# Kernel optimization log

Measured on AMD Instinct MI355X. Metric: run time of the kernel, lower is better.

Reference implementation:

```python
import jax, jax.numpy as jnp
import numpy as np

DIM = 768
NUM_HEADS = 12
HEAD_DIM = DIM // NUM_HEADS
SCALE = HEAD_DIM ** -0.5


def setup_inputs() -> dict:
    key = jax.random.key(0)
    ks = jax.random.split(key, 9)
    B, L, C = 4, 1024, DIM
    x = jax.random.normal(ks[0], (B, L, C), jnp.float32)
    q_ape = jax.random.normal(ks[1], (1, L, C), jnp.float32)
    k_ape = jax.random.normal(ks[2], (1, L, C), jnp.float32)
    attn_pos = jax.random.normal(ks[3], (1, NUM_HEADS, L, L), jnp.float32)
    s = C ** -0.5
    # torch Linear weights: (out_features, in_features)
    Wq = jax.random.normal(ks[4], (C, C), jnp.float32) * s
    Wk = jax.random.normal(ks[5], (C, C), jnp.float32) * s
    Wv = jax.random.normal(ks[6], (C, C), jnp.float32) * s
    Wp = jax.random.normal(ks[7], (C, C), jnp.float32) * s
    bp = jax.random.normal(ks[8], (C,), jnp.float32) * 0.01
    return {"x": x, "q_ape": q_ape, "k_ape": k_ape, "attn_pos": attn_pos,
            "Wq": Wq, "Wk": Wk, "Wv": Wv, "Wp": Wp, "bp": bp}


def _split_heads(t):
    # (B, L, C) -> (B, H, L, D)
    B, L, C = t.shape
    return t.reshape(B, L, NUM_HEADS, HEAD_DIM).transpose(0, 2, 1, 3)


def reference(x, q_ape, k_ape, attn_pos, Wq, Wk, Wv, Wp, bp):
    B, L, C = x.shape
    q = _split_heads((x + q_ape) @ Wq.T)          # (B,H,L,D)
    k = _split_heads((x + k_ape) @ Wk.T)          # (B,H,L,D)
    v = _split_heads(x @ Wv.T)                    # (B,H,L,D)
    attn = jnp.einsum('bhqd,bhkd->bhqk', q, k) * SCALE + attn_pos
    attn = jax.nn.softmax(attn, axis=-1)
    out = jnp.einsum('bhqk,bhkd->bhqd', attn, v)  # (B,H,L,D)
    out = out.transpose(0, 2, 1, 3).reshape(B, L, C)
    return out @ Wp.T + bp
```

## Files before the change

### kernel.cpp

```cpp
#include <hip/hip_runtime.h>
#include <stdint.h>

#define NH 12
#define HD 64
#define NB 4
#define SEQ 1024
#define CDIM 768
#define MTOT (NB*SEQ)
#define MC   (MTOT*CDIM)
#define LC   (SEQ*CDIM)
#define WSZ  (CDIM*CDIM)
#define LST  104
#define EST  136
#define VST  72
#define L2E  1.44269504f
#define BHSZ (SEQ*HD)
#define PTSZ ((size_t)NH*SEQ*SEQ)

typedef __attribute__((ext_vector_type(4))) float f32x4;
typedef __attribute__((ext_vector_type(8))) __bf16 bf16x8;
typedef __attribute__((ext_vector_type(8))) short short8;
typedef __attribute__((ext_vector_type(4))) unsigned short ushort4v;
typedef unsigned short u16;

static __device__ __forceinline__ f32x4 mfma16(short8 a, short8 b, f32x4 c) {
  return __builtin_amdgcn_mfma_f32_16x16x32_bf16(
      __builtin_bit_cast(bf16x8, a), __builtin_bit_cast(bf16x8, b), c, 0, 0, 0);
}
static __device__ __forceinline__ u16 f2bf(float f) {
  unsigned u = __float_as_uint(f);
  u += 0x7FFFu + ((u >> 16) & 1u);
  return (u16)(u >> 16);
}
static __device__ __forceinline__ float bf2f(u16 h) {
  return __uint_as_float(((unsigned)h) << 16);
}
static __device__ __forceinline__ void lds_load16(const void* g, void* l) {
  __builtin_amdgcn_global_load_lds(
      (const __attribute__((address_space(1))) void*)g,
      (__attribute__((address_space(3))) void*)l, 16, 0, 0);
}

#define PREP_BLKS (MC / 4 / 256)
#define CONV_N4   ((4 * WSZ + CDIM) / 4)
#define CONV_BLKS ((CONV_N4 + 255) / 256)
__global__ __launch_bounds__(256) void prep_all(
    const float* __restrict__ xp, const float* __restrict__ qp,
    const float* __restrict__ kp, const float* __restrict__ Wq,
    const float* __restrict__ Wk, const float* __restrict__ Wv,
    const float* __restrict__ Wp, const float* __restrict__ bp,
    u16* __restrict__ Xq, u16* __restrict__ Xk, u16* __restrict__ Xv,
    u16* __restrict__ Wb) {
  int bid = blockIdx.x;
  if (bid < PREP_BLKS) {
    int i4 = bid * 256 + threadIdx.x;
    int a4 = i4 % (LC / 4);
    f32x4 xx = ((const f32x4*)xp)[i4];
    f32x4 qq = ((const f32x4*)qp)[a4];
    f32x4 kk = ((const f32x4*)kp)[a4];
    ushort4v oq, ok, ov;
#pragma unroll
    for (int j = 0; j < 4; j++) {
      oq[j] = f2bf(xx[j] + qq[j]);
      ok[j] = f2bf(xx[j] + kk[j]);
      ov[j] = f2bf(xx[j]);
    }
    ((ushort4v*)Xq)[i4] = oq;
    ((ushort4v*)Xk)[i4] = ok;
    ((ushort4v*)Xv)[i4] = ov;
  } else {
    int i4 = (bid - PREP_BLKS) * 256 + threadIdx.x;
    if (i4 >= CONV_N4) return;
    int sel = i4 / (WSZ / 4);
    int off = i4 - sel * (WSZ / 4);
    const float* src = sel == 0 ? Wq : sel == 1 ? Wk : sel == 2 ? Wv
                     : sel == 3 ? Wp : bp;
    f32x4 v = ((const f32x4*)src)[off];
    ushort4v o;
#pragma unroll
    for (int j = 0; j < 4; j++) o[j] = f2bf(v[j]);
    ((ushort4v*)Wb)[i4] = o;
  }
}

static __device__ __forceinline__ void gemm_core64(
    const u16* __restrict__ Ab, const u16* __restrict__ Wb,
    short* As, short* Bs, f32x4 acc[2][4]) {
  const int t = threadIdx.x;
  const int lane = t & 63, w = t >> 6, quad = lane >> 4, l16 = lane & 15;
  const int wm = (w >> 1) * 32, wn = (w & 1) * 64;
  const int row4 = t >> 2, chunk = (t & 3) * 8;
  for (int k0 = 0; k0 < CDIM; k0 += 64) {
#pragma unroll
    for (int hh = 0; hh < 2; hh++) {
      const u16* ga = Ab + row4 * CDIM + k0 + hh * 32 + chunk;
      const u16* gb = Wb + row4 * CDIM + k0 + hh * 32 + chunk;
      lds_load16(ga,             (char*)As + hh * 4096 + t * 16);
      lds_load16(gb,             (char*)Bs + hh * 8192 + t * 16);
      lds_load16(gb + 64 * CDIM, (char*)Bs + hh * 8192 + 4096 + t * 16);
    }
    __syncthreads();
#pragma unroll
    for (int hh = 0; hh < 2; hh++) {
      const short* Ah = As + hh * 2048;
      const short* Bh = Bs + hh * 4096;
      short8 af[2], bw[4];
#pragma unroll
      for (int i = 0; i < 2; i++)
        af[i] = *(const short8*)(Ah + (wm + i * 16 + l16) * 32 + quad * 8);
#pragma unroll
      for (int j = 0; j < 4; j++)
        bw[j] = *(const short8*)(Bh + (wn + j * 16 + l16) * 32 + quad * 8);
#pragma unroll
      for (int i = 0; i < 2; i++)
#pragma unroll
        for (int j = 0; j < 4; j++)
          acc[i][j] = mfma16(af[i], bw[j], acc[i][j]);
    }
    __syncthreads();
  }
}

__global__ __launch_bounds__(256) void gemm_qkv(
    const u16* __restrict__ Xq, const u16* __restrict__ Xk, const u16* __restrict__ Xv,
    const u16* __restrict__ Wq, const u16* __restrict__ Wk, const u16* __restrict__ Wv,
    u16* __restrict__ Q, u16* __restrict__ K, u16* __restrict__ Vt,
    const float* __restrict__ pos, u16* __restrict__ posT) {
  __shared__ __align__(16) short S[12288];
  const int id = blockIdx.x;
  const int rq = id & 3, qd = id >> 2;
  if (rq == 3) {
    const int t = threadIdx.x, wv = t >> 6, lane = t & 63;
    const int quad = lane >> 4, l16 = lane & 15;
#pragma unroll 1
    for (int c = 0; c < 8; ++c) {
      const int chunk = qd * 32 + wv * 8 + c;
      const int h = chunk >> 10, rem = chunk & 1023;
      const int rb = rem >> 4, kt = rem & 15;
      const float* src = pos + (size_t)h * SEQ * SEQ
                         + (size_t)(rb * 16 + quad * 4) * SEQ + kt * 64 + l16;
      short8 s0, s1;
#pragma unroll
      for (int jj = 0; jj < 2; jj++)
#pragma unroll
        for (int r = 0; r < 4; r++) {
          s0[jj * 4 + r] = (short)f2bf(src[r * SEQ + jj * 16] * L2E);
          s1[jj * 4 + r] = (short)f2bf(src[r * SEQ + (jj + 2) * 16] * L2E);
        }
      u16* dst = posT + (size_t)chunk * 1024 + lane * 16;
      *(short8*)dst = s0;
      *(short8*)(dst + 8) = s1;
    }
    return;
  }

  short* As = S;
  short* Bs = S + 4096;
  const int g = qd * 3 + rq;
  const int z = g / 384, rem = g % 384;
  const int m0 = (rem / 6) * 64, n0 = (rem % 6) * 128;
  const u16* A = (z == 0 ? Xq : z == 1 ? Xk : Xv) + m0 * CDIM;
  const u16* W = (z == 0 ? Wq : z == 1 ? Wk : Wv) + n0 * CDIM;
  f32x4 acc[2][4];
#pragma unroll
  for (int i = 0; i < 2; i++)
#pragma unroll
    for (int j = 0; j < 4; j++) acc[i][j] = 0.f;
  gemm_core64(A, W, As, Bs, acc);

  const int t = threadIdx.x, lane = t & 63, w = t >> 6;
  const int quad = lane >> 4, l16 = lane & 15;
  const int wm = (w >> 1) * 32, wn = (w & 1) * 64;
  const float qs = (z == 0) ? 0.125f : 1.0f;

#pragma unroll
  for (int i = 0; i < 2; i++)
#pragma unroll
    for (int j = 0; j < 4; j++)
#pragma unroll
      for (int r = 0; r < 4; r++) {
        int mr = wm + i * 16 + quad * 4 + r;
        int nc = wn + j * 16 + l16;
        if (z < 2) S[mr * EST + nc] = (short)f2bf(acc[i][j][r] * qs);
        else       S[nc * VST + mr] = (short)f2bf(acc[i][j][r]);
      }
  __syncthreads();

  const int row = t >> 3, ch = t & 7;
  const int b = m0 >> 10, lbase = m0 & 1023;
  if (z == 0) {
#pragma unroll
    for (int cp = 0; cp < 2; cp++) {
      int h = (n0 >> 6) + cp;
#pragma unroll
      for (int rp = 0; rp < 2; rp++) {
        int mr = row + rp * 32;
        short8 v = *(const short8*)(S + mr * EST + cp * 64 + ch * 8);
        *(short8*)(Q + ((((size_t)(b * NH + h)) << 10) + lbase + mr) * HD + ch * 8) = v;
      }
    }
  } else if (z == 1) {
#pragma unroll
    for (int cp = 0; cp < 2; cp++) {
      int h = (n0 >> 6) + cp;
      u16* Kp = K + (size_t)(b * NH + h) * BHSZ;
#pragma unroll
      for (int rp = 0; rp < 2; rp++) {
        int mr = row + rp * 32;
        int tok = lbase + mr;
        short8 v = *(const short8*)(S + mr * EST + cp * 64 + ch * 8);
        *(short8*)(Kp + (((tok >> 4) * 8 + ch) * 16 + (tok & 15)) * 8) = v;
      }
    }
  } else {
#pragma unroll
    for (int rp = 0; rp < 4; rp++) {
      int rn = row + rp * 32;
      int h = (n0 + rn) >> 6, d = rn & 63;
      u16* Vp = Vt + (size_t)(b * NH + h) * BHSZ;
      int jv = d >> 4, ld16 = d & 15;
      int tok = lbase + ch * 8;
      short8 v = *(const short8*)(S + rn * VST + ch * 8);
      *(short8*)(Vp + ((((tok >> 6) * 4 + jv) * 8 + ((tok >> 3) & 7)) * 16 + ld16) * 8) = v;
    }
  }
}

__global__ __launch_bounds__(256, 3) void attn(
    const u16* __restrict__ Q, const u16* __restrict__ Kf, const u16* __restrict__ Vf,
    const u16* __restrict__ posT, u16* __restrict__ O) {
  __shared__ __align__(16) short Ps[4 * 16 * LST];
  const int t = threadIdx.x, lane = t & 63, w = t >> 6;
  const int quad = lane >> 4, l16 = lane & 15;

  const int lid = blockIdx.x;
  const int k8 = lid & 7, m = lid >> 3;
  const int g = k8 * 24 + (m >> 2), b = m & 3;
  const int h = g >> 4, qt = g & 15;
  const int bh = b * NH + h;
  const int q0 = qt * 64 + w * 16;

  const u16* Kg = Kf + (size_t)bh * BHSZ;
  const u16* Vg = Vf + (size_t)bh * BHSZ;
  const u16* Tg = posT + ((size_t)(h * 1024 + (qt * 4 + w) * 16)) * 1024
                  + lane * 16;
  short* Pw = Ps + w * 16 * LST;
  const int fo = quad * 128 + l16 * 8;

  const u16* Qg = Q + ((size_t)bh * SEQ + q0) * HD;
  const short8 qa0 = *(const short8*)(Qg + l16 * HD + quad * 8);
  const short8 qa1 = *(const short8*)(Qg + l16 * HD + 32 + quad * 8);

  f32x4 o[4];
  float lrow[4];
#pragma unroll
  for (int j = 0; j < 4; j++) o[j] = 0.f;
#pragma unroll
  for (int r = 0; r < 4; r++) lrow[r] = 0.f;

  short8 kb0[4], kb1[4];
  short8 pt0, pt1;
#pragma unroll
  for (int j = 0; j < 4; j++) {
    kb0[j] = *(const short8*)(Kg + j * 1024 + fo);
    kb1[j] = *(const short8*)(Kg + j * 1024 + 512 + fo);
  }
  pt0 = *(const short8*)(Tg);
  pt1 = *(const short8*)(Tg + 8);

#pragma unroll 1
  for (int kt = 0; kt < 16; ++kt) {
    const int kbase = kt * 4096;
    short8 vb0[4], vb1[4];
#pragma unroll
    for (int j = 0; j < 4; j++) {
      vb0[j] = *(const short8*)(Vg + kbase + j * 1024 + fo);
      vb1[j] = *(const short8*)(Vg + kbase + j * 1024 + 512 + fo);
    }
    f32x4 s[4];
#pragma unroll
    for (int j = 0; j < 4; j++) {
      f32x4 zz = 0.f;
      s[j] = mfma16(qa1, kb1[j], mfma16(qa0, kb0[j], zz));
    }
#pragma unroll
    for (int j = 0; j < 2; j++)
#pragma unroll
      for (int r = 0; r < 4; r++) {
        float pv = bf2f((u16)pt0[j * 4 + r]);
        float e = __builtin_amdgcn_exp2f(fmaf(s[j][r], L2E, pv));
        unsigned bits = __float_as_uint(e);
        Pw[(quad * 4 + r) * LST + j * 16 + l16] = (short)(bits >> 16);
        lrow[r] += __uint_as_float(bits & 0xFFFF0000u);
      }
#pragma unroll
    for (int j = 2; j < 4; j++)
#pragma unroll
      for (int r = 0; r < 4; r++) {
        float pv = bf2f((u16)pt1[(j - 2) * 4 + r]);
        float e = __builtin_amdgcn_exp2f(fmaf(s[j][r], L2E, pv));
        unsigned bits = __float_as_uint(e);
        Pw[(quad * 4 + r) * LST + j * 16 + l16] = (short)(bits >> 16);
        lrow[r] += __uint_as_float(bits & 0xFFFF0000u);
      }
    if (kt < 15) {
      const int nb = kbase + 4096;
#pragma unroll
      for (int j = 0; j < 4; j++) {
        kb0[j] = *(const short8*)(Kg + nb + j * 1024 + fo);
        kb1[j] = *(const short8*)(Kg + nb + j * 1024 + 512 + fo);
      }
      pt0 = *(const short8*)(Tg + (kt + 1) * 1024);
      pt1 = *(const short8*)(Tg + (kt + 1) * 1024 + 8);
    }
    const short8 pa0 = *(const short8*)(Pw + l16 * LST + quad * 8);
    const short8 pa1 = *(const short8*)(Pw + l16 * LST + 32 + quad * 8);
#pragma unroll
    for (int j = 0; j < 4; j++)
      o[j] = mfma16(pa1, vb1[j], mfma16(pa0, vb0[j], o[j]));
  }

#pragma unroll
  for (int off = 1; off < 16; off <<= 1)
#pragma unroll
    for (int r = 0; r < 4; r++) lrow[r] += __shfl_xor(lrow[r], off);

  u16* Og = O + ((size_t)b * SEQ + q0) * CDIM + h * HD;
  float inv[4];
#pragma unroll
  for (int r = 0; r < 4; r++) inv[r] = 1.0f / lrow[r];
#pragma unroll
  for (int j = 0; j < 4; j++)
#pragma unroll
    for (int r = 0; r < 4; r++)
      Og[(quad * 4 + r) * CDIM + j * 16 + l16] = f2bf(o[j][r] * inv[r]);
}

__global__ __launch_bounds__(256) void gemm_proj(
    const u16* __restrict__ Oin, const u16* __restrict__ Wp,
    const u16* __restrict__ bp, float* __restrict__ out) {
  __shared__ __align__(16) short As[4096], Bs[4096];
  const int t = threadIdx.x;
  const int lane = t & 63, w = t >> 6, quad = lane >> 4, l16 = lane & 15;
  const int wm = (w >> 1) * 32, wn = (w & 1) * 32;
  const int row4 = t >> 2, chunk = (t & 3) * 8;
  const int m0 = blockIdx.y * 64, n0 = blockIdx.x * 64;
  const u16* Ab = Oin + m0 * CDIM;
  const u16* Wb = Wp + n0 * CDIM;
  f32x4 acc[2][2];
#pragma unroll
  for (int i = 0; i < 2; i++)
#pragma unroll
    for (int j = 0; j < 2; j++) acc[i][j] = 0.f;

  for (int k0 = 0; k0 < CDIM; k0 += 64) {
#pragma unroll
    for (int hh = 0; hh < 2; hh++) {
      const u16* ga = Ab + row4 * CDIM + k0 + hh * 32 + chunk;
      const u16* gb = Wb + row4 * CDIM + k0 + hh * 32 + chunk;
      lds_load16(ga, (char*)As + hh * 4096 + t * 16);
      lds_load16(gb, (char*)Bs + hh * 4096 + t * 16);
    }
    __syncthreads();
#pragma unroll
    for (int hh = 0; hh < 2; hh++) {
      const short* Ah = As + hh * 2048;
      const short* Bh = Bs + hh * 2048;
      short8 af[2], bw[2];
#pragma unroll
      for (int i = 0; i < 2; i++)
        af[i] = *(const short8*)(Ah + (wm + i * 16 + l16) * 32 + quad * 8);
#pragma unroll
      for (int j = 0; j < 2; j++)
        bw[j] = *(const short8*)(Bh + (wn + j * 16 + l16) * 32 + quad * 8);
#pragma unroll
      for (int i = 0; i < 2; i++)
#pragma unroll
        for (int j = 0; j < 2; j++)
          acc[i][j] = mfma16(af[i], bw[j], acc[i][j]);
    }
    __syncthreads();
  }

#pragma unroll
  for (int i = 0; i < 2; i++) {
    int mrow = m0 + wm + i * 16 + quad * 4;
#pragma unroll
    for (int j = 0; j < 2; j++) {
      int n = n0 + wn + j * 16 + l16;
      float bias = bf2f(bp[n]);
#pragma unroll
      for (int r = 0; r < 4; r++)
        out[(mrow + r) * CDIM + n] = acc[i][j][r] + bias;
    }
  }
}

extern "C" void kernel_launch(void* const* d_in, const int* in_sizes, int n_in,
                              void* d_out, int out_size, void* d_ws, size_t ws_size,
                              hipStream_t stream) {
  (void)in_sizes; (void)n_in; (void)out_size;
  const size_t OFF_XQ = 0, OFF_XK = (size_t)MC, OFF_XV = 2ull * MC,
               OFF_Q = 3ull * MC, OFF_K = 4ull * MC, OFF_VT = 5ull * MC,
               OFF_W = 6ull * MC, OFF_PT = OFF_W + 4ull * WSZ + 1024,
               TOT = OFF_PT + PTSZ;
  if (ws_size < TOT * sizeof(u16)) return;

  u16* ws = (u16*)d_ws;
  u16 *Xq = ws + OFF_XQ, *Xk = ws + OFF_XK, *Xv = ws + OFF_XV;
  u16 *Qb = ws + OFF_Q, *Kb = ws + OFF_K, *Vt = ws + OFF_VT;
  u16 *Wb = ws + OFF_W, *Pt = ws + OFF_PT;
  u16 *Wqb = Wb, *Wkb = Wb + WSZ, *Wvb = Wb + 2ull * WSZ,
      *Wpb = Wb + 3ull * WSZ, *bpb = Wb + 4ull * WSZ;
  u16* Ob = Xq;

  prep_all<<<PREP_BLKS + CONV_BLKS, 256, 0, stream>>>(
      (const float*)d_in[0], (const float*)d_in[1], (const float*)d_in[2],
      (const float*)d_in[4], (const float*)d_in[5], (const float*)d_in[6],
      (const float*)d_in[7], (const float*)d_in[8], Xq, Xk, Xv, Wb);
  gemm_qkv<<<dim3(1536), 256, 0, stream>>>(Xq, Xk, Xv, Wqb, Wkb, Wvb,
                                           Qb, Kb, Vt,
                                           (const float*)d_in[3], Pt);
  attn<<<dim3(768), 256, 0, stream>>>(Qb, Kb, Vt, Pt, Ob);
  gemm_proj<<<dim3(12, 64), 256, 0, stream>>>(Ob, Wpb, bpb, (float*)d_out);
}
```

Measured before the change: 205.5 us.

## Split attention key range across warp pairs and reduce partials in shared memory

Each attention block now covers 32 queries instead of 64. Two warp halves each process half of the key tiles for the same 16 query rows, and their unnormalised outputs and row sums are combined through shared memory. The grid doubles to 1536 blocks to raise parallelism and shorten the per-warp serial loop. The qkv GEMM grid also changes from an interleaved 1D block-id mapping to a 3D grid, with the pos-transpose blocks on z=3. This loses the previous interleaving of pos-transpose blocks with GEMM blocks, and adds a reduction step plus two block barriers.

```diff
diff --git a/kernel.cpp b/kernel.cpp
--- a/kernel.cpp
+++ b/kernel.cpp
@@ -13,6 +13,7 @@
 #define LST  104
 #define EST  136
 #define VST  72
+#define CST  68
 #define L2E  1.44269504f
 #define BHSZ (SEQ*HD)
 #define PTSZ ((size_t)NH*SEQ*SEQ)
@@ -127,14 +128,13 @@
     u16* __restrict__ Q, u16* __restrict__ K, u16* __restrict__ Vt,
     const float* __restrict__ pos, u16* __restrict__ posT) {
   __shared__ __align__(16) short S[12288];
-  const int id = blockIdx.x;
-  const int rq = id & 3, qd = id >> 2;
-  if (rq == 3) {
+  if (blockIdx.z == 3) {
     const int t = threadIdx.x, wv = t >> 6, lane = t & 63;
+    const int flat = blockIdx.y * 6 + blockIdx.x;
     const int quad = lane >> 4, l16 = lane & 15;
 #pragma unroll 1
     for (int c = 0; c < 8; ++c) {
-      const int chunk = qd * 32 + wv * 8 + c;
+      const int chunk = flat * 32 + wv * 8 + c;
       const int h = chunk >> 10, rem = chunk & 1023;
       const int rb = rem >> 4, kt = rem & 15;
       const float* src = pos + (size_t)h * SEQ * SEQ
@@ -156,9 +156,8 @@
 
   short* As = S;
   short* Bs = S + 4096;
-  const int g = qd * 3 + rq;
-  const int z = g / 384, rem = g % 384;
-  const int m0 = (rem / 6) * 64, n0 = (rem % 6) * 128;
+  const int z = blockIdx.z;
+  const int m0 = blockIdx.y * 64, n0 = blockIdx.x * 128;
   const u16* A = (z == 0 ? Xq : z == 1 ? Xk : Xv) + m0 * CDIM;
   const u16* W = (z == 0 ? Wq : z == 1 ? Wk : Wv) + n0 * CDIM;
   f32x4 acc[2][4];
@@ -232,17 +231,18 @@
   __shared__ __align__(16) short Ps[4 * 16 * LST];
   const int t = threadIdx.x, lane = t & 63, w = t >> 6;
   const int quad = lane >> 4, l16 = lane & 15;
+  const int wsub = w & 1, half = w >> 1;
 
   const int lid = blockIdx.x;
   const int k8 = lid & 7, m = lid >> 3;
-  const int g = k8 * 24 + (m >> 2), b = m & 3;
-  const int h = g >> 4, qt = g & 15;
+  const int g = k8 * 48 + (m >> 2), b = m & 3;
+  const int h = g >> 5, qt = g & 31;
   const int bh = b * NH + h;
-  const int q0 = qt * 64 + w * 16;
+  const int q0 = qt * 32 + wsub * 16;
 
   const u16* Kg = Kf + (size_t)bh * BHSZ;
   const u16* Vg = Vf + (size_t)bh * BHSZ;
-  const u16* Tg = posT + ((size_t)(h * 1024 + (qt * 4 + w) * 16)) * 1024
+  const u16* Tg = posT + ((size_t)(h * 1024 + (qt * 2 + wsub) * 16)) * 1024
                   + lane * 16;
   short* Pw = Ps + w * 16 * LST;
   const int fo = quad * 128 + l16 * 8;
@@ -258,18 +258,20 @@
 #pragma unroll
   for (int r = 0; r < 4; r++) lrow[r] = 0.f;
 
+  const int kt0 = half * 8;
   short8 kb0[4], kb1[4];
   short8 pt0, pt1;
 #pragma unroll
   for (int j = 0; j < 4; j++) {
-    kb0[j] = *(const short8*)(Kg + j * 1024 + fo);
-    kb1[j] = *(const short8*)(Kg + j * 1024 + 512 + fo);
-  }
-  pt0 = *(const short8*)(Tg);
-  pt1 = *(const short8*)(Tg + 8);
+    kb0[j] = *(const short8*)(Kg + kt0 * 4096 + j * 1024 + fo);
+    kb1[j] = *(const short8*)(Kg + kt0 * 4096 + j * 1024 + 512 + fo);
+  }
+  pt0 = *(const short8*)(Tg + kt0 * 1024);
+  pt1 = *(const short8*)(Tg + kt0 * 1024 + 8);
 
 #pragma unroll 1
-  for (int kt = 0; kt < 16; ++kt) {
+  for (int kk = 0; kk < 8; ++kk) {
+    const int kt = kt0 + kk;
     const int kbase = kt * 4096;
     short8 vb0[4], vb1[4];
 #pragma unroll
@@ -303,7 +305,7 @@
         Pw[(quad * 4 + r) * LST + j * 16 + l16] = (short)(bits >> 16);
         lrow[r] += __uint_as_float(bits & 0xFFFF0000u);
       }
-    if (kt < 15) {
+    if (kk < 7) {
       const int nb = kbase + 4096;
 #pragma unroll
       for (int j = 0; j < 4; j++) {
@@ -324,6 +326,30 @@
   for (int off = 1; off < 16; off <<= 1)
 #pragma unroll
     for (int r = 0; r < 4; r++) lrow[r] += __shfl_xor(lrow[r], off);
+
+  __syncthreads();
+  float* Cb = (float*)Ps;
+  const int cb = wsub * (16 * CST + 16);
+  if (half) {
+#pragma unroll
+    for (int j = 0; j < 4; j++)
+#pragma unroll
+      for (int r = 0; r < 4; r++)
+        Cb[cb + (quad * 4 + r) * CST + j * 16 + l16] = o[j][r];
+    if (l16 == 0) {
+#pragma unroll
+      for (int r = 0; r < 4; r++) Cb[cb + 16 * CST + quad * 4 + r] = lrow[r];
+    }
+  }
+  __syncthreads();
+  if (half) return;
+#pragma unroll
+  for (int r = 0; r < 4; r++) lrow[r] += Cb[cb + 16 * CST + quad * 4 + r];
+#pragma unroll
+  for (int j = 0; j < 4; j++)
+#pragma unroll
+    for (int r = 0; r < 4; r++)
+      o[j][r] += Cb[cb + (quad * 4 + r) * CST + j * 16 + l16];
 
   u16* Og = O + ((size_t)b * SEQ + q0) * CDIM + h * HD;
   float inv[4];
@@ -418,9 +444,9 @@
       (const float*)d_in[0], (const float*)d_in[1], (const float*)d_in[2],
       (const float*)d_in[4], (const float*)d_in[5], (const float*)d_in[6],
       (const float*)d_in[7], (const float*)d_in[8], Xq, Xk, Xv, Wb);
-  gemm_qkv<<<dim3(1536), 256, 0, stream>>>(Xq, Xk, Xv, Wqb, Wkb, Wvb,
-                                           Qb, Kb, Vt,
-                                           (const float*)d_in[3], Pt);
-  attn<<<dim3(768), 256, 0, stream>>>(Qb, Kb, Vt, Pt, Ob);
+  gemm_qkv<<<dim3(6, 64, 4), 256, 0, stream>>>(Xq, Xk, Xv, Wqb, Wkb, Wvb,
+                                               Qb, Kb, Vt,
+                                               (const float*)d_in[3], Pt);
+  attn<<<dim3(1536), 256, 0, stream>>>(Qb, Kb, Vt, Pt, Ob);
   gemm_proj<<<dim3(12, 64), 256, 0, stream>>>(Ob, Wpb, bpb, (float*)d_out);
 }
```

Result: faster. 201.3 us (-2.0%).
